# Optimization experiments

Measured on AMD Instinct MI355X. Metric: run time of the kernel, lower is better.

## Reference

```python
import jax, jax.numpy as jnp
import numpy as np

W_PENALTY = 1.0
NUM_CLASSES = 1784
BATCH = 16384


def _build_penalty_matrix(venomous):
    # venomous: [C] int 0/1 per class.
    # Torch loop: row = target class (cls), col = candidate class (c).
    #   c==cls -> 0; (vt=0,vc=0)->1; (vt=0,vc=1)->2; (vt=1,vc=1)->2; (vt=1,vc=0)->5
    M = jnp.asarray([[1.0, 2.0], [5.0, 2.0]], dtype=jnp.float32)  # M[vt, vc]
    P = M[venomous[:, None], venomous[None, :]]  # [C, C]
    P = P * (1.0 - jnp.eye(NUM_CLASSES, dtype=jnp.float32))  # diagonal penalty = 0
    return P


def setup_inputs() -> dict:
    key = jax.random.key(0)
    k1, k2, k3 = jax.random.split(key, 3)
    logits = jax.random.normal(k1, (BATCH, NUM_CLASSES), dtype=jnp.float32)
    targets = jax.random.randint(k2, (BATCH,), 0, NUM_CLASSES, dtype=jnp.int64)
    venomous = jax.random.randint(k3, (NUM_CLASSES,), 0, 2, dtype=jnp.int32)
    penalty_matrix = _build_penalty_matrix(venomous)  # [C, C] float32 constant table
    return {"logits": logits, "targets": targets, "penalty_matrix": penalty_matrix}


def reference(logits, targets, penalty_matrix):
    # per-sample cross entropy (reduction='none')
    logp = jax.nn.log_softmax(logits, axis=-1)  # [B, C]
    ce = -jnp.take_along_axis(logp, targets[:, None], axis=-1)[:, 0]  # [B]
    candidate = jnp.argmax(logits, axis=-1)  # [B]
    penalty = penalty_matrix[targets, candidate]  # [B]
    loss = jnp.sum(ce + penalty * W_PENALTY)
    return loss / targets.shape[0]
```

## Files before the change

kernel.cpp:

```cpp
#include <hip/hip_runtime.h>
#include <math.h>

#define NCLS 1784
#define NF4 446
#define NBATCH 16384
#define NBLOCKS (NBATCH / 4)
#define LOG2E 1.4426950408889634f

__global__ __launch_bounds__(256) void cevp_row_kernel(
        const float* __restrict__ logits,
        const int* __restrict__ targets,
        const float* __restrict__ P,
        float* __restrict__ ws) {
    const int wave = threadIdx.x >> 6;
    const int lane = threadIdx.x & 63;
    const int row  = blockIdx.x * 4 + wave;

    const float4* __restrict__ rp =
        reinterpret_cast<const float4*>(logits + (size_t)row * NCLS);

    float4 v[7];
    #pragma unroll
    for (int k = 0; k < 7; ++k) {
        const int idx = lane + 64 * k;
        if (idx < NF4) {
            v[k] = rp[idx];
        } else {
            v[k] = make_float4(-INFINITY, -INFINITY, -INFINITY, -INFINITY);
        }
    }

    float m = -INFINITY;
    int   mi = NCLS;
    #pragma unroll
    for (int k = 0; k < 7; ++k) {
        const int base = (lane + 64 * k) * 4;
        const float* f = reinterpret_cast<const float*>(&v[k]);
        #pragma unroll
        for (int j = 0; j < 4; ++j) {
            if (f[j] > m) { m = f[j]; mi = base + j; }
        }
    }

    #pragma unroll
    for (int off = 32; off > 0; off >>= 1) {
        const float om = __shfl_xor(m, off, 64);
        const int   oi = __shfl_xor(mi, off, 64);
        if (om > m || (om == m && oi < mi)) { m = om; mi = oi; }
    }

    float s = 0.0f;
    #pragma unroll
    for (int k = 0; k < 7; ++k) {
        const float* f = reinterpret_cast<const float*>(&v[k]);
        #pragma unroll
        for (int j = 0; j < 4; ++j) {
            s += exp2f((f[j] - m) * LOG2E);
        }
    }
    #pragma unroll
    for (int off = 32; off > 0; off >>= 1) {
        s += __shfl_xor(s, off, 64);
    }

    __shared__ float part[4];
    if (lane == 0) {
        const int tgt = targets[row];
        const float lt = logits[(size_t)row * NCLS + tgt];
        const float ce = logf(s) + m - lt;
        const float pen = P[(size_t)tgt * NCLS + mi];
        part[wave] = ce + pen;
    }
    __syncthreads();
    if (threadIdx.x == 0) {
        ws[blockIdx.x] = (part[0] + part[1]) + (part[2] + part[3]);
    }
}

__global__ __launch_bounds__(1024) void cevp_reduce_kernel(
        const float* __restrict__ ws, float* __restrict__ out) {
    __shared__ float sm[16];
    const int tid = threadIdx.x;
    const float4 v = reinterpret_cast<const float4*>(ws)[tid];
    float s = (v.x + v.y) + (v.z + v.w);
    #pragma unroll
    for (int off = 32; off > 0; off >>= 1) {
        s += __shfl_xor(s, off, 64);
    }
    if ((tid & 63) == 0) sm[tid >> 6] = s;
    __syncthreads();
    if (tid < 16) {
        float t = sm[tid];
        #pragma unroll
        for (int off = 8; off > 0; off >>= 1) {
            t += __shfl_xor(t, off, 64);
        }
        if (tid == 0) out[0] = t / (float)NBATCH;
    }
}

extern "C" void kernel_launch(void* const* d_in, const int* in_sizes, int n_in,
                              void* d_out, int out_size, void* d_ws, size_t ws_size,
                              hipStream_t stream) {
    const float* logits  = (const float*)d_in[0];
    const int*   targets = (const int*)d_in[1];
    const float* P       = (const float*)d_in[2];
    float* out = (float*)d_out;
    float* ws  = (float*)d_ws;

    cevp_row_kernel<<<NBLOCKS, 256, 0, stream>>>(logits, targets, P, ws);
    cevp_reduce_kernel<<<1, 1024, 0, stream>>>(ws, out);
}
```

Before: 26.52 us.

## Process two rows per wave with hoisted target loads and split exp accumulators

Each wave now handles two rows, halving the block count and interleaving the loads and reductions of both rows to raise memory-level parallelism. The argmax tracks a compact local slot index that is turned into a column index once before the shuffles, and the target logit and target index loads are issued early. The exp-sum is split into four accumulators per row and uses fmaf to fold the max subtraction. In exchange, register pressure roughly doubles (two 7-float4 buffers per thread), which may lower occupancy.

```diff
diff --git a/kernel.cpp b/kernel.cpp
--- a/kernel.cpp
+++ b/kernel.cpp
@@ -4,7 +4,8 @@
 #define NCLS 1784
 #define NF4 446
 #define NBATCH 16384
-#define NBLOCKS (NBATCH / 4)
+#define ROWS_PER_BLOCK 8
+#define NBLOCKS (NBATCH / ROWS_PER_BLOCK)
 #define LOG2E 1.4426950408889634f
 
 __global__ __launch_bounds__(256) void cevp_row_kernel(
@@ -14,62 +15,91 @@
         float* __restrict__ ws) {
     const int wave = threadIdx.x >> 6;
     const int lane = threadIdx.x & 63;
-    const int row  = blockIdx.x * 4 + wave;
+    const int row0 = blockIdx.x * ROWS_PER_BLOCK + wave * 2;
+    const int row1 = row0 + 1;
 
-    const float4* __restrict__ rp =
-        reinterpret_cast<const float4*>(logits + (size_t)row * NCLS);
+    const int   tgt0 = targets[row0];
+    const int   tgt1 = targets[row1];
+    const float lt0  = logits[(size_t)row0 * NCLS + tgt0];
+    const float lt1  = logits[(size_t)row1 * NCLS + tgt1];
 
-    float4 v[7];
+    const float4* __restrict__ rp0 =
+        reinterpret_cast<const float4*>(logits + (size_t)row0 * NCLS);
+    const float4* __restrict__ rp1 =
+        reinterpret_cast<const float4*>(logits + (size_t)row1 * NCLS);
+
+    float4 a[7], b[7];
     #pragma unroll
     for (int k = 0; k < 7; ++k) {
         const int idx = lane + 64 * k;
-        if (idx < NF4) {
-            v[k] = rp[idx];
-        } else {
-            v[k] = make_float4(-INFINITY, -INFINITY, -INFINITY, -INFINITY);
+        if (idx < NF4) { a[k] = rp0[idx]; b[k] = rp1[idx]; }
+        else {
+            a[k] = make_float4(-INFINITY, -INFINITY, -INFINITY, -INFINITY);
+            b[k] = a[k];
         }
     }
 
-    float m = -INFINITY;
-    int   mi = NCLS;
+    float ma = -INFINITY, mb = -INFINITY;
+    int ca = 0, cb = 0;
     #pragma unroll
     for (int k = 0; k < 7; ++k) {
-        const int base = (lane + 64 * k) * 4;
-        const float* f = reinterpret_cast<const float*>(&v[k]);
+        const float* fa = reinterpret_cast<const float*>(&a[k]);
+        const float* fb = reinterpret_cast<const float*>(&b[k]);
         #pragma unroll
         for (int j = 0; j < 4; ++j) {
-            if (f[j] > m) { m = f[j]; mi = base + j; }
+            const bool ga = fa[j] > ma;
+            ca = ga ? (k * 4 + j) : ca;
+            ma = ga ? fa[j]       : ma;
+            const bool gb = fb[j] > mb;
+            cb = gb ? (k * 4 + j) : cb;
+            mb = gb ? fb[j]       : mb;
         }
     }
+    int ia = ((ca >> 2) << 8) + (lane << 2) + (ca & 3);
+    int ib = ((cb >> 2) << 8) + (lane << 2) + (cb & 3);
 
     #pragma unroll
     for (int off = 32; off > 0; off >>= 1) {
-        const float om = __shfl_xor(m, off, 64);
-        const int   oi = __shfl_xor(mi, off, 64);
-        if (om > m || (om == m && oi < mi)) { m = om; mi = oi; }
+        const float oma = __shfl_xor(ma, off, 64);
+        const int   oia = __shfl_xor(ia, off, 64);
+        if (oma > ma || (oma == ma && oia < ia)) { ma = oma; ia = oia; }
+        const float omb = __shfl_xor(mb, off, 64);
+        const int   oib = __shfl_xor(ib, off, 64);
+        if (omb > mb || (omb == mb && oib < ib)) { mb = omb; ib = oib; }
     }
 
-    float s = 0.0f;
+    const float caon = -ma * LOG2E;
+    const float cbon = -mb * LOG2E;
+    float sa0 = 0.f, sa1 = 0.f, sa2 = 0.f, sa3 = 0.f;
+    float sb0 = 0.f, sb1 = 0.f, sb2 = 0.f, sb3 = 0.f;
     #pragma unroll
     for (int k = 0; k < 7; ++k) {
-        const float* f = reinterpret_cast<const float*>(&v[k]);
-        #pragma unroll
-        for (int j = 0; j < 4; ++j) {
-            s += exp2f((f[j] - m) * LOG2E);
-        }
+        const float* fa = reinterpret_cast<const float*>(&a[k]);
+        const float* fb = reinterpret_cast<const float*>(&b[k]);
+        sa0 += exp2f(fmaf(fa[0], LOG2E, caon));
+        sa1 += exp2f(fmaf(fa[1], LOG2E, caon));
+        sa2 += exp2f(fmaf(fa[2], LOG2E, caon));
+        sa3 += exp2f(fmaf(fa[3], LOG2E, caon));
+        sb0 += exp2f(fmaf(fb[0], LOG2E, cbon));
+        sb1 += exp2f(fmaf(fb[1], LOG2E, cbon));
+        sb2 += exp2f(fmaf(fb[2], LOG2E, cbon));
+        sb3 += exp2f(fmaf(fb[3], LOG2E, cbon));
     }
+    float sa = (sa0 + sa1) + (sa2 + sa3);
+    float sb = (sb0 + sb1) + (sb2 + sb3);
     #pragma unroll
     for (int off = 32; off > 0; off >>= 1) {
-        s += __shfl_xor(s, off, 64);
+        sa += __shfl_xor(sa, off, 64);
+        sb += __shfl_xor(sb, off, 64);
     }
 
     __shared__ float part[4];
     if (lane == 0) {
-        const int tgt = targets[row];
-        const float lt = logits[(size_t)row * NCLS + tgt];
-        const float ce = logf(s) + m - lt;
-        const float pen = P[(size_t)tgt * NCLS + mi];
-        part[wave] = ce + pen;
+        const float ce0  = logf(sa) + ma - lt0;
+        const float pen0 = P[(size_t)tgt0 * NCLS + ia];
+        const float ce1  = logf(sb) + mb - lt1;
+        const float pen1 = P[(size_t)tgt1 * NCLS + ib];
+        part[wave] = (ce0 + pen0) + (ce1 + pen1);
     }
     __syncthreads();
     if (threadIdx.x == 0) {
@@ -77,9 +107,9 @@
     }
 }
 
-__global__ __launch_bounds__(1024) void cevp_reduce_kernel(
+__global__ __launch_bounds__(512) void cevp_reduce_kernel(
         const float* __restrict__ ws, float* __restrict__ out) {
-    __shared__ float sm[16];
+    __shared__ float sm[8];
     const int tid = threadIdx.x;
     const float4 v = reinterpret_cast<const float4*>(ws)[tid];
     float s = (v.x + v.y) + (v.z + v.w);
@@ -89,10 +119,10 @@
     }
     if ((tid & 63) == 0) sm[tid >> 6] = s;
     __syncthreads();
-    if (tid < 16) {
+    if (tid < 8) {
         float t = sm[tid];
         #pragma unroll
-        for (int off = 8; off > 0; off >>= 1) {
+        for (int off = 4; off > 0; off >>= 1) {
             t += __shfl_xor(t, off, 64);
         }
         if (tid == 0) out[0] = t / (float)NBATCH;
@@ -109,5 +139,5 @@
     float* ws  = (float*)d_ws;
 
     cevp_row_kernel<<<NBLOCKS, 256, 0, stream>>>(logits, targets, P, ws);
-    cevp_reduce_kernel<<<1, 1024, 0, stream>>>(ws, out);
+    cevp_reduce_kernel<<<1, 512, 0, stream>>>(ws, out);
 }
```

Result: slower. 27.83 us (+4.9%).
